# Kernel optimization log

Measured on AMD Instinct MI355X. Metric: run time of the kernel, lower is better.

Reference implementation:

```python
import jax, jax.numpy as jnp
import numpy as np

N, D = 2048, 1024
H, KV, HD = 16, 4, 64
REPEATS = H // KV
SCALE = HD ** -0.5


def setup_inputs() -> dict:
    key = jax.random.key(0)
    ks = jax.random.split(key, 6)
    x = jax.random.normal(ks[0], (N, D), dtype=jnp.float32)
    # rotary tables: cos/sin of interleaved-pair angles (llama-style view_as_complex)
    pos = jnp.arange(N, dtype=jnp.float32)[:, None]
    inv_freq = 1.0 / (10000.0 ** (jnp.arange(0, HD, 2, dtype=jnp.float32) / HD))
    ang = pos * inv_freq[None, :]  # (N, HD//2)
    freqs_cos = jnp.cos(ang)
    freqs_sin = jnp.sin(ang)
    s = 0.02
    Wq = jax.random.normal(ks[1], (D, H * HD), dtype=jnp.float32) * s
    Wk = jax.random.normal(ks[2], (D, KV * HD), dtype=jnp.float32) * s
    Wv = jax.random.normal(ks[3], (D, KV * HD), dtype=jnp.float32) * s
    Wo = jax.random.normal(ks[4], (H * HD, D), dtype=jnp.float32) * s
    return {"x": x, "freqs_cos": freqs_cos, "freqs_sin": freqs_sin,
            "Wq": Wq, "Wk": Wk, "Wv": Wv, "Wo": Wo}


def _rope(t, cos, sin):
    # t: (N, heads, HD); interleaved complex pairs (even=real, odd=imag)
    tr = t[..., 0::2]
    ti = t[..., 1::2]
    c = cos[:, None, :]
    s = sin[:, None, :]
    out_r = tr * c - ti * s
    out_i = tr * s + ti * c
    return jnp.stack([out_r, out_i], axis=-1).reshape(t.shape)


def reference(x, freqs_cos, freqs_sin, Wq, Wk, Wv, Wo):
    n = x.shape[0]
    xq = (x @ Wq).reshape(n, H, HD)
    xk = (x @ Wk).reshape(n, KV, HD)
    xv = (x @ Wv).reshape(n, KV, HD)
    xq = _rope(xq, freqs_cos, freqs_sin)
    xk = _rope(xk, freqs_cos, freqs_sin)
    # repeat_kv along head dim (GQA)
    k = jnp.repeat(xk, REPEATS, axis=1)  # (n, H, HD)
    v = jnp.repeat(xv, REPEATS, axis=1)
    # memory_efficient_attention with mask=None: full attention over token axis
    scores = jnp.einsum('nhd,mhd->hnm', xq, k) * SCALE
    attn = jax.nn.softmax(scores, axis=-1)
    out = jnp.einsum('hnm,mhd->nhd', attn, v)
    return out.reshape(n, H * HD) @ Wo
```

## Files before the change

### kernel.cpp

```cpp
#include <hip/hip_runtime.h>

#define N_TOK 2048
#define DMODEL 1024
#define NH 16
#define NKV 4
#define HDIM 64
#define SCALE_LOG2E 0.1803368801111204f

typedef __attribute__((ext_vector_type(8))) short short8;
typedef __attribute__((ext_vector_type(4))) float f32x4;
typedef unsigned short u16;
typedef unsigned int u32;

__device__ __forceinline__ u16 f2bf(float x) {
    u32 u = __float_as_uint(x);
    u += 0x7FFF + ((u >> 16) & 1);
    return (u16)(u >> 16);
}
__device__ __forceinline__ u32 pack2(float a, float b) {
    return (u32)f2bf(a) | ((u32)f2bf(b) << 16);
}
__device__ __forceinline__ u32 pack2t(float a, float b) {
    return __builtin_amdgcn_perm(__float_as_uint(b), __float_as_uint(a), 0x07060302u);
}

__global__ __launch_bounds__(256) void prep(
    const float* __restrict__ Wq, const float* __restrict__ Wk,
    const float* __restrict__ Wv, const float* __restrict__ Wo,
    const float* __restrict__ x,
    u16* __restrict__ Wqt, u16* __restrict__ Wkt, u16* __restrict__ Wvt,
    u16* __restrict__ Wot, u16* __restrict__ xb)
{
    const int z = blockIdx.z;
    const int t = threadIdx.x;
    if (z == 4) {
        size_t base = ((size_t)(blockIdx.y * 16 + blockIdx.x)) * 8192;
#pragma unroll
        for (int i = 0; i < 8; ++i) {
            float4 v = *(const float4*)(x + base + i * 1024 + t * 4);
            uint2 p; p.x = pack2(v.x, v.y); p.y = pack2(v.z, v.w);
            *(uint2*)(xb + base + i * 1024 + t * 4) = p;
        }
        return;
    }
    const float* W; u16* Wt; int NC;
    if      (z == 0) { W = Wq; Wt = Wqt; NC = 1024; }
    else if (z == 1) { W = Wk; Wt = Wkt; NC = 256; }
    else if (z == 2) { W = Wv; Wt = Wvt; NC = 256; }
    else             { W = Wo; Wt = Wot; NC = 1024; }
    const int n0 = blockIdx.x * 64;
    if (n0 >= NC) return;
    const int k0 = blockIdx.y * 64;
    __shared__ float T[64][68];
    const int row = t >> 2, cs = (t & 3) * 16;
#pragma unroll
    for (int i = 0; i < 4; ++i)
        *(float4*)&T[row][cs + i * 4] =
            *(const float4*)(W + (size_t)(k0 + row) * NC + n0 + cs + i * 4);
    __syncthreads();
    const int nl = t >> 2, ks = (t & 3) * 16;
    u32 pk[8];
#pragma unroll
    for (int i = 0; i < 8; ++i)
        pk[i] = pack2(T[ks + 2 * i][nl], T[ks + 2 * i + 1][nl]);
    u16* dst = Wt + (size_t)(n0 + nl) * DMODEL + k0 + ks;
    uint4 w0; w0.x = pk[0]; w0.y = pk[1]; w0.z = pk[2]; w0.w = pk[3];
    uint4 w1; w1.x = pk[4]; w1.y = pk[5]; w1.z = pk[6]; w1.w = pk[7];
    *(uint4*)(dst) = w0;
    *(uint4*)(dst + 8) = w1;
}

__global__ __launch_bounds__(256, 3) void gemm_qkv(
    const u16* __restrict__ A,
    const u16* __restrict__ B0, const u16* __restrict__ B1, const u16* __restrict__ B2,
    u16* __restrict__ D0, u16* __restrict__ D1, u16* __restrict__ FVout,
    const float* __restrict__ fc, const float* __restrict__ fs)
{
    __shared__ u16 As[64][40];
    __shared__ u16 Bs[64][40];
    const int t = threadIdx.x;
    const int m0 = blockIdx.x * 64;
    const int by = blockIdx.y;

    const u16* Bt; int nl0, ep;
    u16* dbf = nullptr; int dstride = 0; float epsc = 1.f;
    if (by < 16)      { Bt = B0; nl0 = by * 64;        dbf = D0; ep = 1; dstride = 1024;
                        epsc = SCALE_LOG2E; }
    else if (by < 20) { Bt = B1; nl0 = (by - 16) * 64; dbf = D1; ep = 1; dstride = 256; }
    else              { Bt = B2; nl0 = (by - 20) * 64; ep = 2; }

    const int w = t >> 6, lane = t & 63;
    const int quad = lane >> 4, l15 = lane & 15;
    const int wm = (w >> 1) * 32, wn = (w & 1) * 32;
    const int srow = t >> 2, sk = (t & 3) * 8;

    const u16* Ap = A + (size_t)(m0 + srow) * DMODEL + sk;
    const u16* Bp = Bt + (size_t)(nl0 + srow) * DMODEL + sk;

    f32x4 acc[2][2];
#pragma unroll
    for (int i = 0; i < 2; ++i)
#pragma unroll
        for (int j = 0; j < 2; ++j) acc[i][j] = {0.f, 0.f, 0.f, 0.f};

    uint4 ar = *(const uint4*)(Ap);
    uint4 br = *(const uint4*)(Bp);

    for (int k0 = 0; k0 < DMODEL; k0 += 32) {
        __syncthreads();
        *(uint4*)&As[srow][sk] = ar;
        *(uint4*)&Bs[srow][sk] = br;
        __syncthreads();
        if (k0 + 32 < DMODEL) {
            ar = *(const uint4*)(Ap + k0 + 32);
            br = *(const uint4*)(Bp + k0 + 32);
        }
        short8 af[2], bf[2];
#pragma unroll
        for (int i = 0; i < 2; ++i)
            af[i] = *(const short8*)&As[wm + i * 16 + l15][quad * 8];
#pragma unroll
        for (int j = 0; j < 2; ++j)
            bf[j] = *(const short8*)&Bs[wn + j * 16 + l15][quad * 8];
#pragma unroll
        for (int i = 0; i < 2; ++i)
#pragma unroll
            for (int j = 0; j < 2; ++j)
                acc[i][j] = __builtin_amdgcn_mfma_f32_16x16x32_bf16(af[i], bf[j], acc[i][j], 0, 0, 0);
    }

#pragma unroll
    for (int i = 0; i < 2; ++i)
#pragma unroll
        for (int j = 0; j < 2; ++j) {
            const int cl = nl0 + wn + j * 16 + l15;
#pragma unroll
            for (int r4 = 0; r4 < 4; ++r4) {
                const int r = m0 + wm + i * 16 + quad * 4 + r4;
                float own = acc[i][j][r4];
                if (ep == 1) {
                    float other = __shfl_xor(own, 1, 64);
                    const int p = (cl & 63) >> 1;
                    const float c = fc[r * 32 + p] * epsc, s = fs[r * 32 + p] * epsc;
                    float outv = ((cl & 1) == 0) ? (own * c - other * s)
                                                 : (other * s + own * c);
                    dbf[(size_t)r * dstride + cl] = f2bf(outv);
                } else {
                    const int g = cl >> 6, d = cl & 63;
                    const int dt = d >> 4, l15v = d & 15;
                    const int kt = r >> 6, klo = r & 63;
                    const int c = klo >> 5, k5 = klo & 31;
                    const int qd = k5 >> 3, jv = k5 & 7;
                    size_t idx = ((((size_t)(g * 32 + kt) * 4 + dt) * 2 + c) * 64
                                  + qd * 16 + l15v) * 8 + jv;
                    FVout[idx] = f2bf(own);
                }
            }
        }
}

__global__ __launch_bounds__(256, 2) void gemm_out(
    const u16* __restrict__ A, const u16* __restrict__ Bt, float* __restrict__ Dout)
{
    __shared__ u16 As[64][40];
    __shared__ u16 Bs[64][40];
    const int t = threadIdx.x;
    const int m0 = blockIdx.x * 64;
    const int nl0 = blockIdx.y * 64;

    const int w = t >> 6, lane = t & 63;
    const int quad = lane >> 4, l15 = lane & 15;
    const int wm = (w >> 1) * 32, wn = (w & 1) * 32;
    const int srow = t >> 2, sk = (t & 3) * 8;

    const u16* Ap = A + (size_t)(m0 + srow) * DMODEL + sk;
    const u16* Bp = Bt + (size_t)(nl0 + srow) * DMODEL + sk;

    f32x4 acc[2][2];
#pragma unroll
    for (int i = 0; i < 2; ++i)
#pragma unroll
        for (int j = 0; j < 2; ++j) acc[i][j] = {0.f, 0.f, 0.f, 0.f};

    uint4 ar = *(const uint4*)(Ap);
    uint4 br = *(const uint4*)(Bp);

    for (int k0 = 0; k0 < DMODEL; k0 += 32) {
        __syncthreads();
        *(uint4*)&As[srow][sk] = ar;
        *(uint4*)&Bs[srow][sk] = br;
        __syncthreads();
        if (k0 + 32 < DMODEL) {
            ar = *(const uint4*)(Ap + k0 + 32);
            br = *(const uint4*)(Bp + k0 + 32);
        }
        short8 af[2], bf[2];
#pragma unroll
        for (int i = 0; i < 2; ++i)
            af[i] = *(const short8*)&As[wm + i * 16 + l15][quad * 8];
#pragma unroll
        for (int j = 0; j < 2; ++j)
            bf[j] = *(const short8*)&Bs[wn + j * 16 + l15][quad * 8];
#pragma unroll
        for (int i = 0; i < 2; ++i)
#pragma unroll
            for (int j = 0; j < 2; ++j)
                acc[i][j] = __builtin_amdgcn_mfma_f32_16x16x32_bf16(af[i], bf[j], acc[i][j], 0, 0, 0);
    }

#pragma unroll
    for (int i = 0; i < 2; ++i)
#pragma unroll
        for (int j = 0; j < 2; ++j) {
            const int cl = nl0 + wn + j * 16 + l15;
#pragma unroll
            for (int r4 = 0; r4 < 4; ++r4) {
                const int r = m0 + wm + i * 16 + quad * 4 + r4;
                Dout[(size_t)r * 1024 + cl] = acc[i][j][r4];
            }
        }
}

__global__ __launch_bounds__(256, 2) void attn(
    const u16* __restrict__ Qb, const u16* __restrict__ Kb,
    const u16* __restrict__ FV, u16* __restrict__ Ob)
{
    __shared__ u16 Ks[2][128][72];
    __shared__ u16 Ps[4][2][16][68];

    const int t = threadIdx.x;
    const int n0 = blockIdx.x * 64;
    const int h = blockIdx.y, kvh = h >> 2;
    const int w = t >> 6, lane = t & 63;
    const int quad = lane >> 4, l15 = lane & 15;
    const int srow = t >> 1, ssel = (t & 1) * 32;

    const u16* qp = Qb + (size_t)(n0 + w * 16 + l15) * (NH * HDIM) + h * HDIM + quad * 8;
    const short8 aq0 = *(const short8*)qp;
    const short8 aq1 = *(const short8*)(qp + 32);

    const u16* kbase = Kb + (size_t)srow * (NKV * HDIM) + kvh * HDIM + ssel;
    const u16* fvb = FV + ((size_t)kvh * 32 * 4096) + (size_t)lane * 8;

    f32x4 o[4];
#pragma unroll
    for (int i = 0; i < 4; ++i) o[i] = {0.f, 0.f, 0.f, 0.f};
    float l_acc = 0.f;

#pragma unroll
    for (int c = 0; c < 4; ++c)
        *(uint4*)&Ks[0][srow][ssel + c * 8] = *(const uint4*)(kbase + c * 8);
    __syncthreads();

    for (int rd = 0; rd < 16; ++rd) {
        const int cur = rd & 1, nxt = cur ^ 1;
        const int rdn = (rd + 1) & 15;
        uint4 kr[4];
#pragma unroll
        for (int c = 0; c < 4; ++c)
            kr[c] = *(const uint4*)(kbase + (size_t)(rdn * 128) * (NKV * HDIM) + c * 8);

#pragma unroll
        for (int sub = 0; sub < 2; ++sub) {
            const int kt = rd * 2 + sub;
            short8 vf0[4], vf1[4];
#pragma unroll
            for (int dt = 0; dt < 4; ++dt) {
                vf0[dt] = *(const short8*)(fvb + (size_t)kt * 4096 + (dt * 2 + 0) * 512);
                vf1[dt] = *(const short8*)(fvb + (size_t)kt * 4096 + (dt * 2 + 1) * 512);
            }
            f32x4 s[4];
#pragma unroll
            for (int nt = 0; nt < 4; ++nt) {
                short8 kb0 = *(const short8*)&Ks[cur][sub * 64 + nt * 16 + l15][quad * 8];
                short8 kb1 = *(const short8*)&Ks[cur][sub * 64 + nt * 16 + l15][quad * 8 + 32];
                f32x4 z = {0.f, 0.f, 0.f, 0.f};
                z = __builtin_amdgcn_mfma_f32_16x16x32_bf16(kb0, aq0, z, 0, 0, 0);
                z = __builtin_amdgcn_mfma_f32_16x16x32_bf16(kb1, aq1, z, 0, 0, 0);
                s[nt] = z;
            }
#pragma unroll
            for (int nt = 0; nt < 4; ++nt) {
                float p0 = __builtin_amdgcn_exp2f(s[nt][0]);
                float p1 = __builtin_amdgcn_exp2f(s[nt][1]);
                float p2 = __builtin_amdgcn_exp2f(s[nt][2]);
                float p3 = __builtin_amdgcn_exp2f(s[nt][3]);
                l_acc += (p0 + p1) + (p2 + p3);
                uint2 pk; pk.x = pack2t(p0, p1); pk.y = pack2t(p2, p3);
                *(uint2*)&Ps[w][sub][l15][nt * 16 + quad * 4] = pk;
            }
            const short8 ap0 = *(const short8*)&Ps[w][sub][l15][quad * 8];
            const short8 ap1 = *(const short8*)&Ps[w][sub][l15][quad * 8 + 32];
#pragma unroll
            for (int dt = 0; dt < 4; ++dt) {
                o[dt] = __builtin_amdgcn_mfma_f32_16x16x32_bf16(ap0, vf0[dt], o[dt], 0, 0, 0);
                o[dt] = __builtin_amdgcn_mfma_f32_16x16x32_bf16(ap1, vf1[dt], o[dt], 0, 0, 0);
            }
        }
#pragma unroll
        for (int c = 0; c < 4; ++c)
            *(uint4*)&Ks[nxt][srow][ssel + c * 8] = kr[c];
        __syncthreads();
    }

    l_acc += __shfl_xor(l_acc, 16, 64);
    l_acc += __shfl_xor(l_acc, 32, 64);
    float linv[4];
#pragma unroll
    for (int r = 0; r < 4; ++r)
        linv[r] = 1.f / __shfl(l_acc, quad * 4 + r, 16);
#pragma unroll
    for (int dt = 0; dt < 4; ++dt)
#pragma unroll
        for (int r = 0; r < 4; ++r) {
            const int qrow = n0 + w * 16 + quad * 4 + r;
            const int col = h * HDIM + dt * 16 + l15;
            Ob[(size_t)qrow * (NH * HDIM) + col] = f2bf(o[dt][r] * linv[r]);
        }
}

extern "C" void kernel_launch(void* const* d_in, const int* in_sizes, int n_in,
                              void* d_out, int out_size, void* d_ws, size_t ws_size,
                              hipStream_t stream) {
    const float* x  = (const float*)d_in[0];
    const float* fc = (const float*)d_in[1];
    const float* fs = (const float*)d_in[2];
    const float* Wq = (const float*)d_in[3];
    const float* Wk = (const float*)d_in[4];
    const float* Wv = (const float*)d_in[5];
    const float* Wo = (const float*)d_in[6];
    float* out = (float*)d_out;

    u16* ws  = (u16*)d_ws;
    u16* xb  = ws;
    u16* Wqt = xb  + (size_t)2048 * 1024;
    u16* Wkt = Wqt + (size_t)1024 * 1024;
    u16* Wvt = Wkt + (size_t)256 * 1024;
    u16* Wot = Wvt + (size_t)256 * 1024;
    u16* qb  = Wot + (size_t)1024 * 1024;
    u16* kb  = qb  + (size_t)2048 * 1024;
    u16* fv  = kb  + (size_t)2048 * 256;
    u16* aob = fv  + (size_t)256 * 2048;

    prep<<<dim3(16, 16, 5), dim3(256), 0, stream>>>(Wq, Wk, Wv, Wo, x,
                                                    Wqt, Wkt, Wvt, Wot, xb);
    gemm_qkv<<<dim3(32, 24), dim3(256), 0, stream>>>(xb, Wqt, Wkt, Wvt,
                                                     qb, kb, fv, fc, fs);
    attn<<<dim3(32, 16), dim3(256), 0, stream>>>(qb, kb, fv, aob);
    gemm_out<<<dim3(32, 16), dim3(256), 0, stream>>>(aob, Wot, out);
}
```

Measured before the change: 140.2 us.

## Switch attention to 32x32 MFMA tiles with a two-way key split and combine pass

The attention kernel now uses 32x32x16 bf16 MFMA with 128 query rows per block instead of 16x16x32 tiles over 64 rows. The key axis is split across two blocks in grid z, so the grid keeps the same block count. Each half writes unnormalized fp32 partial outputs and row sums, and a new combine kernel adds them, normalizes and packs to bf16. The V pre-layout in the QKV GEMM epilogue is rewritten to match the new fragment order. The goal is more MFMA work per LDS and fragment load, at the cost of an extra launch and about 16 MB of fp32 partial traffic.

```diff
diff --git a/kernel.cpp b/kernel.cpp
--- a/kernel.cpp
+++ b/kernel.cpp
@@ -9,6 +9,7 @@
 
 typedef __attribute__((ext_vector_type(8))) short short8;
 typedef __attribute__((ext_vector_type(4))) float f32x4;
+typedef __attribute__((ext_vector_type(16))) float f32x16;
 typedef unsigned short u16;
 typedef unsigned int u32;
 
@@ -147,12 +148,11 @@
                     dbf[(size_t)r * dstride + cl] = f2bf(outv);
                 } else {
                     const int g = cl >> 6, d = cl & 63;
-                    const int dt = d >> 4, l15v = d & 15;
-                    const int kt = r >> 6, klo = r & 63;
-                    const int c = klo >> 5, k5 = klo & 31;
-                    const int qd = k5 >> 3, jv = k5 & 7;
-                    size_t idx = ((((size_t)(g * 32 + kt) * 4 + dt) * 2 + c) * 64
-                                  + qd * 16 + l15v) * 8 + jv;
+                    const int d2 = d >> 5, dl = d & 31;
+                    const int keyblk = r >> 7, kg = (r >> 5) & 3;
+                    const int kst = (r >> 4) & 1, hb = (r >> 3) & 1, jv = r & 7;
+                    size_t idx = ((((((size_t)(g * 16 + keyblk) * 4 + kg) * 2 + kst) * 2 + d2)
+                                   * 2 + hb) * 32 + dl) * 8 + jv;
                     FVout[idx] = f2bf(own);
                 }
             }
@@ -221,30 +221,34 @@
         }
 }
 
-__global__ __launch_bounds__(256, 2) void attn(
+__global__ __launch_bounds__(256, 2) void attn_part(
     const u16* __restrict__ Qb, const u16* __restrict__ Kb,
-    const u16* __restrict__ FV, u16* __restrict__ Ob)
+    const u16* __restrict__ FV, float* __restrict__ Opart, float* __restrict__ Lpart)
 {
     __shared__ u16 Ks[2][128][72];
-    __shared__ u16 Ps[4][2][16][68];
+    __shared__ u16 Ps[4][32][40];
 
     const int t = threadIdx.x;
-    const int n0 = blockIdx.x * 64;
+    const int n0 = blockIdx.x * 128;
     const int h = blockIdx.y, kvh = h >> 2;
+    const int ksp = blockIdx.z;
     const int w = t >> 6, lane = t & 63;
-    const int quad = lane >> 4, l15 = lane & 15;
+    const int hi = lane >> 5, l31 = lane & 31;
     const int srow = t >> 1, ssel = (t & 1) * 32;
 
-    const u16* qp = Qb + (size_t)(n0 + w * 16 + l15) * (NH * HDIM) + h * HDIM + quad * 8;
-    const short8 aq0 = *(const short8*)qp;
-    const short8 aq1 = *(const short8*)(qp + 32);
-
-    const u16* kbase = Kb + (size_t)srow * (NKV * HDIM) + kvh * HDIM + ssel;
-    const u16* fvb = FV + ((size_t)kvh * 32 * 4096) + (size_t)lane * 8;
-
-    f32x4 o[4];
-#pragma unroll
-    for (int i = 0; i < 4; ++i) o[i] = {0.f, 0.f, 0.f, 0.f};
+    const u16* qp = Qb + (size_t)(n0 + w * 32 + l31) * (NH * HDIM) + h * HDIM + hi * 8;
+    short8 qf[4];
+#pragma unroll
+    for (int s = 0; s < 4; ++s) qf[s] = *(const short8*)(qp + s * 16);
+
+    const u16* kbase = Kb + (size_t)(ksp * 1024 + srow) * (NKV * HDIM) + kvh * HDIM + ssel;
+    const u16* fvb = FV + ((size_t)kvh * 16 * 8192) + (size_t)lane * 8;
+
+    f32x16 o[2];
+#pragma unroll
+    for (int d2 = 0; d2 < 2; ++d2)
+#pragma unroll
+        for (int r = 0; r < 16; ++r) o[d2][r] = 0.f;
     float l_acc = 0.f;
 
 #pragma unroll
@@ -252,49 +256,50 @@
         *(uint4*)&Ks[0][srow][ssel + c * 8] = *(const uint4*)(kbase + c * 8);
     __syncthreads();
 
-    for (int rd = 0; rd < 16; ++rd) {
+    for (int rd = 0; rd < 8; ++rd) {
         const int cur = rd & 1, nxt = cur ^ 1;
-        const int rdn = (rd + 1) & 15;
+        const int rdn = (rd + 1) & 7;
         uint4 kr[4];
 #pragma unroll
         for (int c = 0; c < 4; ++c)
             kr[c] = *(const uint4*)(kbase + (size_t)(rdn * 128) * (NKV * HDIM) + c * 8);
-
-#pragma unroll
-        for (int sub = 0; sub < 2; ++sub) {
-            const int kt = rd * 2 + sub;
-            short8 vf0[4], vf1[4];
-#pragma unroll
-            for (int dt = 0; dt < 4; ++dt) {
-                vf0[dt] = *(const short8*)(fvb + (size_t)kt * 4096 + (dt * 2 + 0) * 512);
-                vf1[dt] = *(const short8*)(fvb + (size_t)kt * 4096 + (dt * 2 + 1) * 512);
-            }
-            f32x4 s[4];
-#pragma unroll
-            for (int nt = 0; nt < 4; ++nt) {
-                short8 kb0 = *(const short8*)&Ks[cur][sub * 64 + nt * 16 + l15][quad * 8];
-                short8 kb1 = *(const short8*)&Ks[cur][sub * 64 + nt * 16 + l15][quad * 8 + 32];
-                f32x4 z = {0.f, 0.f, 0.f, 0.f};
-                z = __builtin_amdgcn_mfma_f32_16x16x32_bf16(kb0, aq0, z, 0, 0, 0);
-                z = __builtin_amdgcn_mfma_f32_16x16x32_bf16(kb1, aq1, z, 0, 0, 0);
-                s[nt] = z;
-            }
-#pragma unroll
-            for (int nt = 0; nt < 4; ++nt) {
-                float p0 = __builtin_amdgcn_exp2f(s[nt][0]);
-                float p1 = __builtin_amdgcn_exp2f(s[nt][1]);
-                float p2 = __builtin_amdgcn_exp2f(s[nt][2]);
-                float p3 = __builtin_amdgcn_exp2f(s[nt][3]);
-                l_acc += (p0 + p1) + (p2 + p3);
-                uint2 pk; pk.x = pack2t(p0, p1); pk.y = pack2t(p2, p3);
-                *(uint2*)&Ps[w][sub][l15][nt * 16 + quad * 4] = pk;
-            }
-            const short8 ap0 = *(const short8*)&Ps[w][sub][l15][quad * 8];
-            const short8 ap1 = *(const short8*)&Ps[w][sub][l15][quad * 8 + 32];
-#pragma unroll
-            for (int dt = 0; dt < 4; ++dt) {
-                o[dt] = __builtin_amdgcn_mfma_f32_16x16x32_bf16(ap0, vf0[dt], o[dt], 0, 0, 0);
-                o[dt] = __builtin_amdgcn_mfma_f32_16x16x32_bf16(ap1, vf1[dt], o[dt], 0, 0, 0);
+        const int keyblk = ksp * 8 + rd;
+
+#pragma unroll
+        for (int kg = 0; kg < 4; ++kg) {
+            short8 vf[2][2];
+#pragma unroll
+            for (int s = 0; s < 2; ++s)
+#pragma unroll
+                for (int d2 = 0; d2 < 2; ++d2)
+                    vf[s][d2] = *(const short8*)(fvb +
+                        ((((size_t)keyblk * 4 + kg) * 2 + s) * 2 + d2) * 512);
+            f32x16 sa;
+#pragma unroll
+            for (int r = 0; r < 16; ++r) sa[r] = 0.f;
+#pragma unroll
+            for (int s = 0; s < 4; ++s) {
+                short8 kf = *(const short8*)&Ks[cur][kg * 32 + l31][s * 16 + hi * 8];
+                sa = __builtin_amdgcn_mfma_f32_32x32x16_bf16(kf, qf[s], sa, 0, 0, 0);
+            }
+            float p[16];
+#pragma unroll
+            for (int r = 0; r < 16; ++r) p[r] = __builtin_amdgcn_exp2f(sa[r]);
+            l_acc += ((p[0] + p[1]) + (p[2] + p[3])) + ((p[4] + p[5]) + (p[6] + p[7]))
+                   + ((p[8] + p[9]) + (p[10] + p[11])) + ((p[12] + p[13]) + (p[14] + p[15]));
+#pragma unroll
+            for (int blk = 0; blk < 4; ++blk) {
+                uint2 pk;
+                pk.x = pack2t(p[blk * 4 + 0], p[blk * 4 + 1]);
+                pk.y = pack2t(p[blk * 4 + 2], p[blk * 4 + 3]);
+                *(uint2*)&Ps[w][l31][blk * 8 + 4 * hi] = pk;
+            }
+            const short8 ap0 = *(const short8*)&Ps[w][l31][hi * 8];
+            const short8 ap1 = *(const short8*)&Ps[w][l31][16 + hi * 8];
+#pragma unroll
+            for (int d2 = 0; d2 < 2; ++d2) {
+                o[d2] = __builtin_amdgcn_mfma_f32_32x32x16_bf16(ap0, vf[0][d2], o[d2], 0, 0, 0);
+                o[d2] = __builtin_amdgcn_mfma_f32_32x32x16_bf16(ap1, vf[1][d2], o[d2], 0, 0, 0);
             }
         }
 #pragma unroll
@@ -303,20 +308,32 @@
         __syncthreads();
     }
 
-    l_acc += __shfl_xor(l_acc, 16, 64);
     l_acc += __shfl_xor(l_acc, 32, 64);
-    float linv[4];
-#pragma unroll
-    for (int r = 0; r < 4; ++r)
-        linv[r] = 1.f / __shfl(l_acc, quad * 4 + r, 16);
-#pragma unroll
-    for (int dt = 0; dt < 4; ++dt)
-#pragma unroll
-        for (int r = 0; r < 4; ++r) {
-            const int qrow = n0 + w * 16 + quad * 4 + r;
-            const int col = h * HDIM + dt * 16 + l15;
-            Ob[(size_t)qrow * (NH * HDIM) + col] = f2bf(o[dt][r] * linv[r]);
-        }
+    if (lane < 32)
+        Lpart[(size_t)ksp * (NH * N_TOK) + h * N_TOK + n0 + w * 32 + lane] = l_acc;
+    float* op = Opart + (size_t)ksp * N_TOK * 1024;
+#pragma unroll
+    for (int d2 = 0; d2 < 2; ++d2)
+#pragma unroll
+        for (int r = 0; r < 16; ++r) {
+            const int q = n0 + w * 32 + (r & 3) + 8 * (r >> 2) + 4 * hi;
+            op[(size_t)q * 1024 + h * HDIM + d2 * 32 + l31] = o[d2][r];
+        }
+}
+
+__global__ __launch_bounds__(256) void combine(
+    const float* __restrict__ Opart, const float* __restrict__ Lpart,
+    u16* __restrict__ aob)
+{
+    const int row = blockIdx.x, t = threadIdx.x;
+    const int h = t >> 4;
+    const float4 a = *(const float4*)(Opart + (size_t)row * 1024 + t * 4);
+    const float4 b = *(const float4*)(Opart + (size_t)N_TOK * 1024 + (size_t)row * 1024 + t * 4);
+    const float li = 1.f / (Lpart[h * N_TOK + row] + Lpart[NH * N_TOK + h * N_TOK + row]);
+    uint2 ov;
+    ov.x = pack2((a.x + b.x) * li, (a.y + b.y) * li);
+    ov.y = pack2((a.z + b.z) * li, (a.w + b.w) * li);
+    *(uint2*)(aob + (size_t)row * 1024 + t * 4) = ov;
 }
 
 extern "C" void kernel_launch(void* const* d_in, const int* in_sizes, int n_in,
@@ -341,11 +358,14 @@
     u16* kb  = qb  + (size_t)2048 * 1024;
     u16* fv  = kb  + (size_t)2048 * 256;
     u16* aob = fv  + (size_t)256 * 2048;
+    float* opart = (float*)(aob + (size_t)2048 * 1024);
+    float* lpart = opart + (size_t)2 * 2048 * 1024;
 
     prep<<<dim3(16, 16, 5), dim3(256), 0, stream>>>(Wq, Wk, Wv, Wo, x,
                                                     Wqt, Wkt, Wvt, Wot, xb);
     gemm_qkv<<<dim3(32, 24), dim3(256), 0, stream>>>(xb, Wqt, Wkt, Wvt,
                                                      qb, kb, fv, fc, fs);
-    attn<<<dim3(32, 16), dim3(256), 0, stream>>>(qb, kb, fv, aob);
+    attn_part<<<dim3(16, 16, 2), dim3(256), 0, stream>>>(qb, kb, fv, opart, lpart);
+    combine<<<dim3(2048), dim3(256), 0, stream>>>(opart, lpart, aob);
     gemm_out<<<dim3(32, 16), dim3(256), 0, stream>>>(aob, Wot, out);
 }
```

New measurement: 138.1 us. About the same (-1.5%).
